# Kernel optimization log

Measured on AMD Instinct MI355X. Metric: run time of the kernel, lower is better.

Reference implementation:

```python
import jax, jax.numpy as jnp
import numpy as np
import math

B, SQ, SK = 8, 1024, 1024
DIM_Q = DIM_K = DIM_V = 512
H = 8
EPS = 1e-5
INF = jnp.float32(1e38)


def _ln(x, g, b):
    mu = jnp.mean(x, axis=-1, keepdims=True)
    var = jnp.mean(jnp.square(x - mu), axis=-1, keepdims=True)
    return (x - mu) * jax.lax.rsqrt(var + EPS) * g + b


def setup_inputs() -> dict:
    key = jax.random.key(0)
    ks = jax.random.split(key, 12)
    s = 1.0 / math.sqrt(DIM_V)
    return {
        "queries": jax.random.normal(ks[0], (B, SQ, DIM_Q), jnp.float32),
        "keys": jax.random.normal(ks[1], (B, SK, DIM_K), jnp.float32),
        # binary presence masks (as in the original usage)
        "presence_q": (jax.random.uniform(ks[2], (B, SQ)) > 0.1).astype(jnp.float32),
        "presence_k": (jax.random.uniform(ks[3], (B, SK)) > 0.1).astype(jnp.float32),
        "num_heads": H,
        "Wq": jax.random.normal(ks[4], (DIM_Q, DIM_V), jnp.float32) * s,
        "bq": jnp.zeros((DIM_V,), jnp.float32),
        "Wk": jax.random.normal(ks[5], (DIM_K, DIM_V), jnp.float32) * s,
        "bk": jnp.zeros((DIM_V,), jnp.float32),
        "Wv": jax.random.normal(ks[6], (DIM_K, DIM_V), jnp.float32) * s,
        "bv": jnp.zeros((DIM_V,), jnp.float32),
        "Wo": jax.random.normal(ks[7], (DIM_V, DIM_V), jnp.float32) * s,
        "bo": jnp.zeros((DIM_V,), jnp.float32),
        "g0": jnp.ones((DIM_V,), jnp.float32),
        "b0": jnp.zeros((DIM_V,), jnp.float32),
        "g1": jnp.ones((DIM_V,), jnp.float32),
        "b1": jnp.zeros((DIM_V,), jnp.float32),
    }


def reference(queries, keys, presence_q, presence_k, num_heads,
              Wq, bq, Wk, bk, Wv, bv, Wo, bo, g0, b0, g1, b1):
    b, sq, _ = queries.shape
    dim_v = Wq.shape[1]
    d = dim_v // num_heads
    q = queries @ Wq + bq                              # [B,Sq,V]
    k = keys @ Wk + bk                                 # [B,Sk,V]
    v = keys @ Wv + bv                                 # [B,Sk,V]
    qh = q.reshape(b, sq, num_heads, d)
    kh = k.reshape(b, -1, num_heads, d)
    vh = v.reshape(b, -1, num_heads, d)
    logits = jnp.einsum('bqhd,bkhd->bhqk', qh, kh) / jnp.float32(math.sqrt(dim_v))
    pq = presence_q[:, None, :, None]                  # [B,1,Sq,1]
    logits = pq * logits - (1.0 - pq) * INF
    pk = presence_k[:, None, None, :]                  # [B,1,1,Sk]
    logits = pk * logits - (1.0 - pk) * INF
    A = jax.nn.softmax(logits, axis=-1)                # [B,H,Sq,Sk]
    o = qh + jnp.einsum('bhqk,bkhd->bqhd', A, vh)      # residual add of Q_
    o = o.reshape(b, sq, dim_v)
    o = _ln(o, g0, b0)
    o = o + jax.nn.relu(o @ Wo + bo)
    o = _ln(o, g1, b1)
    return o
```

## Files before the change

### kernel.cpp

```cpp
#include <hip/hip_runtime.h>

typedef __attribute__((ext_vector_type(8))) short short8;
typedef __attribute__((ext_vector_type(4))) float f32x4;

#define SCALE2 0.06375871571f
#define C1     674.4237f

__device__ __forceinline__ float bfu(unsigned short u){
  return __uint_as_float(((unsigned int)u) << 16);
}
__device__ __forceinline__ unsigned short f2b(float x){
  unsigned int b = __float_as_uint(x);
  return (unsigned short)((b + 0x7fffu + ((b>>16)&1u)) >> 16);
}
__device__ __forceinline__ uint4 pack8(const float* f){
  float4 a = *(const float4*)f, b = *(const float4*)(f+4);
  uint4 r;
  r.x = (unsigned)f2b(a.x) | ((unsigned)f2b(a.y)<<16);
  r.y = (unsigned)f2b(a.z) | ((unsigned)f2b(a.w)<<16);
  r.z = (unsigned)f2b(b.x) | ((unsigned)f2b(b.y)<<16);
  r.w = (unsigned)f2b(b.z) | ((unsigned)f2b(b.w)<<16);
  return r;
}

__global__ __launch_bounds__(256) void conv_bf(
    const float* q, const float* k, unsigned short* dst)
{
  long i = ((long)blockIdx.x*256 + threadIdx.x)*8;
  const float* src = (i < 4194304) ? q + i : k + (i - 4194304);
  *(uint4*)(dst + i) = pack8(src);
}

__global__ __launch_bounds__(256) void prep_w(
    const float* Wq, const float* Wk, const float* Wv, const float* Wo,
    unsigned short* wt)
{
  const int m = blockIdx.z;
  const float* W = (m==0)?Wq:(m==1)?Wk:(m==2)?Wv:Wo;
  unsigned short* dst = wt + (long)m*262144;
  __shared__ unsigned short tile[64][72];
  const int t = threadIdx.x;
  const int n0 = blockIdx.x*64, k0 = blockIdx.y*64;
  {
    int r = t>>2, c0 = (t&3)*16;
    uint4 u0 = pack8(W + (long)(k0+r)*512 + n0 + c0);
    uint4 u1 = pack8(W + (long)(k0+r)*512 + n0 + c0 + 8);
    unsigned short* us0 = (unsigned short*)&u0;
    unsigned short* us1 = (unsigned short*)&u1;
    #pragma unroll
    for (int i=0;i<8;++i) tile[c0+i][r] = us0[i];
    #pragma unroll
    for (int i=0;i<8;++i) tile[c0+8+i][r] = us1[i];
  }
  __syncthreads();
  {
    int n = t>>2, ks = (t&3)*16;
    *(uint4*)(dst + (long)(n0+n)*512 + k0 + ks)     = *(uint4*)&tile[n][ks];
    *(uint4*)(dst + (long)(n0+n)*512 + k0 + ks + 8) = *(uint4*)&tile[n][ks+8];
  }
}

__global__ __launch_bounds__(256) void proj_mfma(
    const unsigned short* qin, const unsigned short* kin, const unsigned short* wt,
    const float* bq, const float* bk, const float* bv,
    unsigned short* q_bf, unsigned short* k_bf, unsigned short* vt_bf)
{
  const int mat = blockIdx.z;
  const unsigned short* A = (mat==0)? qin : kin;
  const unsigned short* Wt = wt + (long)mat*262144;
  const float* bias = (mat==0)?bq:(mat==1)?bk:bv;
  const int row0 = blockIdx.y*128, col0 = blockIdx.x*128;
  __shared__ unsigned short As[2][128][40];
  __shared__ unsigned short Ws[2][128][40];
  const int t = threadIdx.x;
  const int lane = t & 63, wid = t >> 6;
  const int ln = lane & 15, quad = lane >> 4;
  const int wy = wid >> 1, wx = wid & 1;
  f32x4 acc[4][4];
  #pragma unroll
  for (int i=0;i<4;++i){
    #pragma unroll
    for (int j=0;j<4;++j) acc[i][j] = (f32x4){0.f,0.f,0.f,0.f};
  }
  const int sr = t>>1, sk0 = (t&1)*16;
  const unsigned short* Arow = A  + (long)(row0+sr)*512 + sk0;
  const unsigned short* Wrow = Wt + (long)(col0+sr)*512 + sk0;
  uint4 a0 = *(const uint4*)(Arow);
  uint4 a1 = *(const uint4*)(Arow + 8);
  uint4 w0 = *(const uint4*)(Wrow);
  uint4 w1 = *(const uint4*)(Wrow + 8);
  *(uint4*)&As[0][sr][sk0]   = a0;
  *(uint4*)&As[0][sr][sk0+8] = a1;
  *(uint4*)&Ws[0][sr][sk0]   = w0;
  *(uint4*)&Ws[0][sr][sk0+8] = w1;
  __syncthreads();
  for (int it=0; it<16; ++it){
    const int cur = it & 1;
    if (it < 15){
      a0 = *(const uint4*)(Arow + (it+1)*32);
      a1 = *(const uint4*)(Arow + (it+1)*32 + 8);
      w0 = *(const uint4*)(Wrow + (it+1)*32);
      w1 = *(const uint4*)(Wrow + (it+1)*32 + 8);
    }
    short8 a[4], b[4];
    #pragma unroll
    for (int mt=0;mt<4;++mt) a[mt] = *(const short8*)&As[cur][wy*64+mt*16+ln][quad*8];
    #pragma unroll
    for (int nt=0;nt<4;++nt) b[nt] = *(const short8*)&Ws[cur][wx*64+nt*16+ln][quad*8];
    #pragma unroll
    for (int mt=0;mt<4;++mt){
      #pragma unroll
      for (int nt=0;nt<4;++nt)
        acc[mt][nt] = __builtin_amdgcn_mfma_f32_16x16x32_bf16(a[mt], b[nt], acc[mt][nt], 0,0,0);
    }
    if (it < 15){
      *(uint4*)&As[cur^1][sr][sk0]   = a0;
      *(uint4*)&As[cur^1][sr][sk0+8] = a1;
      *(uint4*)&Ws[cur^1][sr][sk0]   = w0;
      *(uint4*)&Ws[cur^1][sr][sk0+8] = w1;
    }
    __syncthreads();
  }
  float bias_v[4];
  #pragma unroll
  for (int nt=0;nt<4;++nt) bias_v[nt] = bias[col0 + wx*64 + nt*16 + ln];
  if (mat < 2){
    unsigned short* dst = (mat==0)? q_bf : k_bf;
    #pragma unroll
    for (int mt=0;mt<4;++mt){
      int row = row0 + wy*64 + mt*16 + quad*4;
      #pragma unroll
      for (int nt=0;nt<4;++nt){
        int col = col0 + wx*64 + nt*16 + ln;
        #pragma unroll
        for (int r=0;r<4;++r)
          dst[(long)(row+r)*512 + col] = f2b(acc[mt][nt][r] + bias_v[nt]);
      }
    }
  } else {
    #pragma unroll
    for (int mt=0;mt<4;++mt){
      int row = row0 + wy*64 + mt*16 + quad*4;
      int bb = row >> 10, sk = row & 1023;
      #pragma unroll
      for (int nt=0;nt<4;++nt){
        int col = col0 + wx*64 + nt*16 + ln;
        int h = col >> 6, dd = col & 63;
        uint2 pk2; unsigned short* pp = (unsigned short*)&pk2;
        #pragma unroll
        for (int r=0;r<4;++r) pp[r] = f2b(acc[mt][nt][r] + bias_v[nt]);
        *(uint2*)(vt_bf + (((long)((bb*8+h)*64+dd)) << 10) + sk) = pk2;
      }
    }
  }
}

__global__ __launch_bounds__(512) void attn_mfma(
    const unsigned short* q_bf, const unsigned short* k_bf, const unsigned short* vt_bf,
    const float* pres_q, const float* pres_k, float* o1)
{
  const int bx = blockIdx.x;
  const int b = bx >> 3, h = bx & 7;
  const int q0 = blockIdx.y * 128;
  const int t = threadIdx.x;
  const int lane = t & 63, wid = t >> 6, ln = lane & 15, quad = lane >> 4;
  __shared__ unsigned short Qs[128][72];
  __shared__ unsigned short Ks[64][72];
  __shared__ unsigned short Vt[64][72];
  __shared__ unsigned short Ps[128][72];
  __shared__ float pq_s[128], pk_s[64];
  {
    int tok = t>>2, ds = (t&3)*16;
    const unsigned short* src = q_bf + (long)(b*1024 + q0 + tok)*512 + h*64 + ds;
    *(uint4*)&Qs[tok][ds]   = *(const uint4*)src;
    *(uint4*)&Qs[tok][ds+8] = *(const uint4*)(src+8);
  }
  if (t < 128) pq_s[t] = pres_q[b*1024 + q0 + t];
  __syncthreads();
  short8 aq0 = *(const short8*)&Qs[wid*16+ln][quad*8];
  short8 aq1 = *(const short8*)&Qs[wid*16+ln][32+quad*8];
  float av[4];
  #pragma unroll
  for (int r=0;r<4;++r) av[r] = pq_s[wid*16 + quad*4 + r]*SCALE2;
  f32x4 oacc[4];
  #pragma unroll
  for (int dt=0;dt<4;++dt) oacc[dt] = (f32x4){0.f,0.f,0.f,0.f};
  float lsum[4] = {0.f,0.f,0.f,0.f};

  for (int k0=0;k0<1024;k0+=64){
    __syncthreads();
    {
      int tok = t>>3, ds = (t&7)*8;
      *(uint4*)&Ks[tok][ds] = *(const uint4*)(k_bf + (long)(b*1024 + k0 + tok)*512 + h*64 + ds);
      *(uint4*)&Vt[tok][ds] = *(const uint4*)(vt_bf + (((long)((b*8+h)*64 + tok)) << 10) + k0 + ds);
    }
    if (t < 64) pk_s[t] = pres_k[b*1024 + k0 + t];
    __syncthreads();
    f32x4 s[4];
    #pragma unroll
    for (int kt=0;kt<4;++kt) s[kt] = (f32x4){0.f,0.f,0.f,0.f};
    #pragma unroll
    for (int kt=0;kt<4;++kt){
      short8 kb0 = *(const short8*)&Ks[kt*16+ln][quad*8];
      short8 kb1 = *(const short8*)&Ks[kt*16+ln][32+quad*8];
      s[kt] = __builtin_amdgcn_mfma_f32_16x16x32_bf16(aq0, kb0, s[kt], 0,0,0);
      s[kt] = __builtin_amdgcn_mfma_f32_16x16x32_bf16(aq1, kb1, s[kt], 0,0,0);
    }
    float pk4[4];
    #pragma unroll
    for (int kt=0;kt<4;++kt) pk4[kt] = pk_s[kt*16+ln];
    #pragma unroll
    for (int r=0;r<4;++r){
      float sv[4];
      #pragma unroll
      for (int kt=0;kt<4;++kt){
        float a = av[r]*pk4[kt];
        float c = __builtin_fmaf(a, C1, -43.f);
        float x = __builtin_fmaf(s[kt][r], a, c);
        x = fminf(fmaxf(x, -100.f), 60.f);
        float e = __builtin_amdgcn_exp2f(x);
        lsum[r] += e;
        sv[kt] = e;
      }
      int prow = wid*16 + quad*4 + r;
      #pragma unroll
      for (int kt=0;kt<4;++kt) Ps[prow][kt*16+ln] = f2b(sv[kt]);
    }
    short8 ap0 = *(const short8*)&Ps[wid*16+ln][quad*8];
    short8 ap1 = *(const short8*)&Ps[wid*16+ln][32+quad*8];
    #pragma unroll
    for (int dt=0;dt<4;++dt){
      short8 vb0 = *(const short8*)&Vt[dt*16+ln][quad*8];
      short8 vb1 = *(const short8*)&Vt[dt*16+ln][32+quad*8];
      oacc[dt] = __builtin_amdgcn_mfma_f32_16x16x32_bf16(ap0, vb0, oacc[dt], 0,0,0);
      oacc[dt] = __builtin_amdgcn_mfma_f32_16x16x32_bf16(ap1, vb1, oacc[dt], 0,0,0);
    }
  }
  #pragma unroll
  for (int r=0;r<4;++r){
    float l = lsum[r];
    #pragma unroll
    for (int msk=1; msk<16; msk<<=1) l += __shfl_xor(l, msk);
    float inv = 1.f / l;
    int ql = wid*16 + quad*4 + r;
    long base = (long)(b*1024 + q0 + ql)*512 + h*64;
    #pragma unroll
    for (int dt=0;dt<4;++dt)
      o1[base + dt*16 + ln] = bfu(Qs[ql][dt*16+ln]) + oacc[dt][r]*inv;
  }
}

__global__ __launch_bounds__(256) void ln_kernel(
    const float* in, void* outp, int mode, const float* g, const float* bvec)
{
  const int row = blockIdx.x*4 + (threadIdx.x >> 6);
  const int lane = threadIdx.x & 63;
  const float* x = in + (long)row*512 + lane*8;
  float v[8];
  *(float4*)&v[0] = *(const float4*)x;
  *(float4*)&v[4] = *(const float4*)(x + 4);
  float sum = 0.f;
  #pragma unroll
  for (int c=0;c<8;++c) sum += v[c];
  #pragma unroll
  for (int msk=1; msk<64; msk<<=1) sum += __shfl_xor(sum, msk);
  float mu = sum * (1.f/512.f);
  float var = 0.f;
  #pragma unroll
  for (int c=0;c<8;++c){ v[c] -= mu; var += v[c]*v[c]; }
  #pragma unroll
  for (int msk=1; msk<64; msk<<=1) var += __shfl_xor(var, msk);
  float rs = rsqrtf(var*(1.f/512.f) + 1e-5f);
  float gv[8], bv[8];
  *(float4*)&gv[0] = *(const float4*)(g + lane*8);
  *(float4*)&gv[4] = *(const float4*)(g + lane*8 + 4);
  *(float4*)&bv[0] = *(const float4*)(bvec + lane*8);
  *(float4*)&bv[4] = *(const float4*)(bvec + lane*8 + 4);
  float y[8];
  #pragma unroll
  for (int c=0;c<8;++c) y[c] = v[c]*rs*gv[c] + bv[c];
  if (mode){
    float* dst = (float*)outp + (long)row*512 + lane*8;
    *(float4*)dst       = *(float4*)&y[0];
    *(float4*)(dst + 4) = *(float4*)&y[4];
  } else {
    uint4 out; unsigned short* os = (unsigned short*)&out;
    #pragma unroll
    for (int c=0;c<8;++c) os[c] = f2b(y[c]);
    *(uint4*)((unsigned short*)outp + (long)row*512 + lane*8) = out;
  }
}

__global__ __launch_bounds__(256) void out_mfma(
    const unsigned short* t_bf, const unsigned short* Wt, const float* bo,
    float* o1)
{
  const int row0 = blockIdx.y*64, col0 = blockIdx.x*128;
  __shared__ unsigned short As[2][64][40];
  __shared__ unsigned short Ws[2][128][40];
  const int t = threadIdx.x;
  const int lane = t & 63, wid = t >> 6;
  const int ln = lane & 15, quad = lane >> 4;
  const int wy = wid >> 1, wx = wid & 1;
  f32x4 acc[2][4];
  #pragma unroll
  for (int i=0;i<2;++i){
    #pragma unroll
    for (int j=0;j<4;++j) acc[i][j] = (f32x4){0.f,0.f,0.f,0.f};
  }
  const int ar = t>>2, ac0 = (t&3)*8;
  const int wr = t>>1, wc0 = (t&1)*16;
  const unsigned short* Arow = t_bf + (long)(row0+ar)*512 + ac0;
  const unsigned short* Wrow = Wt   + (long)(col0+wr)*512 + wc0;
  uint4 a0 = *(const uint4*)(Arow);
  uint4 w0 = *(const uint4*)(Wrow);
  uint4 w1 = *(const uint4*)(Wrow + 8);
  *(uint4*)&As[0][ar][ac0] = a0;
  *(uint4*)&Ws[0][wr][wc0]   = w0;
  *(uint4*)&Ws[0][wr][wc0+8] = w1;
  __syncthreads();
  for (int it=0; it<16; ++it){
    const int cur = it & 1;
    if (it < 15){
      a0 = *(const uint4*)(Arow + (it+1)*32);
      w0 = *(const uint4*)(Wrow + (it+1)*32);
      w1 = *(const uint4*)(Wrow + (it+1)*32 + 8);
    }
    short8 a[2], b[4];
    #pragma unroll
    for (int mt=0;mt<2;++mt) a[mt] = *(const short8*)&As[cur][wy*32+mt*16+ln][quad*8];
    #pragma unroll
    for (int nt=0;nt<4;++nt) b[nt] = *(const short8*)&Ws[cur][wx*64+nt*16+ln][quad*8];
    #pragma unroll
    for (int mt=0;mt<2;++mt){
      #pragma unroll
      for (int nt=0;nt<4;++nt)
        acc[mt][nt] = __builtin_amdgcn_mfma_f32_16x16x32_bf16(a[mt], b[nt], acc[mt][nt], 0,0,0);
    }
    if (it < 15){
      *(uint4*)&As[cur^1][ar][ac0] = a0;
      *(uint4*)&Ws[cur^1][wr][wc0]   = w0;
      *(uint4*)&Ws[cur^1][wr][wc0+8] = w1;
    }
    __syncthreads();
  }
  float bias_v[4];
  #pragma unroll
  for (int nt=0;nt<4;++nt) bias_v[nt] = bo[col0 + wx*64 + nt*16 + ln];
  #pragma unroll
  for (int mt=0;mt<2;++mt){
    int row = row0 + wy*32 + mt*16 + quad*4;
    #pragma unroll
    for (int nt=0;nt<4;++nt){
      int col = col0 + wx*64 + nt*16 + ln;
      #pragma unroll
      for (int r=0;r<4;++r){
        long idx = (long)(row+r)*512 + col;
        float u = acc[mt][nt][r] + bias_v[nt];
        u = fmaxf(u, 0.f);
        o1[idx] = bfu(t_bf[idx]) + u;
      }
    }
  }
}

extern "C" void kernel_launch(void* const* d_in, const int* in_sizes, int n_in,
                              void* d_out, int out_size, void* d_ws, size_t ws_size,
                              hipStream_t stream)
{
  unsigned short* q_bf  = (unsigned short*)d_ws;
  unsigned short* k_bf  = q_bf  + 8192l*512;
  unsigned short* vt_bf = k_bf  + 8192l*512;
  unsigned short* t_bf  = vt_bf + 8192l*512;
  unsigned short* wt    = t_bf  + 8192l*512;
  float* o1 = (float*)(wt + 4l*512*512);
  unsigned short* qin = (unsigned short*)o1;
  unsigned short* kin = qin + 4194304;

  hipLaunchKernelGGL(conv_bf, dim3(4096), dim3(256), 0, stream,
                     (const float*)d_in[0], (const float*)d_in[1], qin);
  hipLaunchKernelGGL(prep_w, dim3(8,8,4), dim3(256), 0, stream,
                     (const float*)d_in[5], (const float*)d_in[7],
                     (const float*)d_in[9], (const float*)d_in[11], wt);
  hipLaunchKernelGGL(proj_mfma, dim3(4,64,3), dim3(256), 0, stream,
                     qin, kin, wt,
                     (const float*)d_in[6], (const float*)d_in[8],
                     (const float*)d_in[10], q_bf, k_bf, vt_bf);
  hipLaunchKernelGGL(attn_mfma, dim3(64,8), dim3(512), 0, stream,
                     q_bf, k_bf, vt_bf,
                     (const float*)d_in[2], (const float*)d_in[3], o1);
  hipLaunchKernelGGL(ln_kernel, dim3(2048), dim3(256), 0, stream,
                     o1, (void*)t_bf, 0, (const float*)d_in[13], (const float*)d_in[14]);
  hipLaunchKernelGGL(out_mfma, dim3(4,128), dim3(256), 0, stream,
                     t_bf, wt + 3l*512*512, (const float*)d_in[12], o1);
  hipLaunchKernelGGL(ln_kernel, dim3(2048), dim3(256), 0, stream,
                     o1, d_out, 1, (const float*)d_in[15], (const float*)d_in[16]);
}
```

Baseline: 213.4 us.

## Double-buffer attention K/V, bf16 intermediates, merge prep kernels, simplify softmax math

Merges the input-conversion and weight-transpose kernels into a single launch. The attention kernel now double-buffers K/V tiles with register prefetch, so it needs one barrier per iteration instead of two. It also reuses the Q shared buffer for P, simplifies the fixed-offset softmax exponent, and truncates P to bf16 instead of rounding it. The intermediates between attention, LayerNorm and the output projection are stored as bf16 instead of fp32, which halves that memory traffic but adds rounding error before each LayerNorm. The clamp on the exponent is removed and the residual Q is read from global memory, and both changes slightly alter numerical behaviour.

```diff
diff --git a/kernel.cpp b/kernel.cpp
--- a/kernel.cpp
+++ b/kernel.cpp
@@ -4,7 +4,6 @@
 typedef __attribute__((ext_vector_type(4))) float f32x4;
 
 #define SCALE2 0.06375871571f
-#define C1     674.4237f
 
 __device__ __forceinline__ float bfu(unsigned short u){
   return __uint_as_float(((unsigned int)u) << 16);
@@ -23,40 +22,38 @@
   return r;
 }
 
-__global__ __launch_bounds__(256) void conv_bf(
-    const float* q, const float* k, unsigned short* dst)
-{
-  long i = ((long)blockIdx.x*256 + threadIdx.x)*8;
-  const float* src = (i < 4194304) ? q + i : k + (i - 4194304);
-  *(uint4*)(dst + i) = pack8(src);
-}
-
-__global__ __launch_bounds__(256) void prep_w(
+__global__ __launch_bounds__(256) void prep_inputs(
     const float* Wq, const float* Wk, const float* Wv, const float* Wo,
-    unsigned short* wt)
-{
-  const int m = blockIdx.z;
-  const float* W = (m==0)?Wq:(m==1)?Wk:(m==2)?Wv:Wo;
-  unsigned short* dst = wt + (long)m*262144;
-  __shared__ unsigned short tile[64][72];
-  const int t = threadIdx.x;
-  const int n0 = blockIdx.x*64, k0 = blockIdx.y*64;
-  {
-    int r = t>>2, c0 = (t&3)*16;
-    uint4 u0 = pack8(W + (long)(k0+r)*512 + n0 + c0);
-    uint4 u1 = pack8(W + (long)(k0+r)*512 + n0 + c0 + 8);
-    unsigned short* us0 = (unsigned short*)&u0;
-    unsigned short* us1 = (unsigned short*)&u1;
-    #pragma unroll
-    for (int i=0;i<8;++i) tile[c0+i][r] = us0[i];
-    #pragma unroll
-    for (int i=0;i<8;++i) tile[c0+8+i][r] = us1[i];
-  }
-  __syncthreads();
-  {
-    int n = t>>2, ks = (t&3)*16;
-    *(uint4*)(dst + (long)(n0+n)*512 + k0 + ks)     = *(uint4*)&tile[n][ks];
-    *(uint4*)(dst + (long)(n0+n)*512 + k0 + ks + 8) = *(uint4*)&tile[n][ks+8];
+    const float* q, const float* k, unsigned short* wt, unsigned short* qk_dst)
+{
+  const int id = blockIdx.x, t = threadIdx.x;
+  if (id < 256){
+    const int m = id >> 6;
+    const float* W = (m==0)?Wq:(m==1)?Wk:(m==2)?Wv:Wo;
+    unsigned short* dst = wt + (long)m*262144;
+    __shared__ unsigned short tile[64][72];
+    const int n0 = ((id>>3)&7)*64, k0 = (id&7)*64;
+    {
+      int r = t>>2, c0 = (t&3)*16;
+      uint4 u0 = pack8(W + (long)(k0+r)*512 + n0 + c0);
+      uint4 u1 = pack8(W + (long)(k0+r)*512 + n0 + c0 + 8);
+      unsigned short* us0 = (unsigned short*)&u0;
+      unsigned short* us1 = (unsigned short*)&u1;
+      #pragma unroll
+      for (int i=0;i<8;++i) tile[c0+i][r] = us0[i];
+      #pragma unroll
+      for (int i=0;i<8;++i) tile[c0+8+i][r] = us1[i];
+    }
+    __syncthreads();
+    {
+      int n = t>>2, ks = (t&3)*16;
+      *(uint4*)(dst + (long)(n0+n)*512 + k0 + ks)     = *(uint4*)&tile[n][ks];
+      *(uint4*)(dst + (long)(n0+n)*512 + k0 + ks + 8) = *(uint4*)&tile[n][ks+8];
+    }
+  } else {
+    long i = ((long)(id-256)*256 + t)*8;
+    const float* src = (i < 4194304) ? q + i : k + (i - 4194304);
+    *(uint4*)(qk_dst + i) = pack8(src);
   }
 }
 
@@ -157,84 +154,95 @@
 
 __global__ __launch_bounds__(512) void attn_mfma(
     const unsigned short* q_bf, const unsigned short* k_bf, const unsigned short* vt_bf,
-    const float* pres_q, const float* pres_k, float* o1)
+    const float* pres_q, const float* pres_k, unsigned short* o_bf)
 {
   const int bx = blockIdx.x;
   const int b = bx >> 3, h = bx & 7;
   const int q0 = blockIdx.y * 128;
   const int t = threadIdx.x;
   const int lane = t & 63, wid = t >> 6, ln = lane & 15, quad = lane >> 4;
-  __shared__ unsigned short Qs[128][72];
-  __shared__ unsigned short Ks[64][72];
-  __shared__ unsigned short Vt[64][72];
-  __shared__ unsigned short Ps[128][72];
-  __shared__ float pq_s[128], pk_s[64];
+  __shared__ unsigned short QP[128][72];
+  __shared__ unsigned short Ks[2][64][72];
+  __shared__ unsigned short Vt[2][64][72];
+  __shared__ float pq_s[128];
+  __shared__ float pk_s[2][64];
   {
     int tok = t>>2, ds = (t&3)*16;
     const unsigned short* src = q_bf + (long)(b*1024 + q0 + tok)*512 + h*64 + ds;
-    *(uint4*)&Qs[tok][ds]   = *(const uint4*)src;
-    *(uint4*)&Qs[tok][ds+8] = *(const uint4*)(src+8);
+    *(uint4*)&QP[tok][ds]   = *(const uint4*)src;
+    *(uint4*)&QP[tok][ds+8] = *(const uint4*)(src+8);
+  }
+  {
+    int tok = t>>3, ds = (t&7)*8;
+    *(uint4*)&Ks[0][tok][ds] = *(const uint4*)(k_bf + (long)(b*1024 + tok)*512 + h*64 + ds);
+    *(uint4*)&Vt[0][tok][ds] = *(const uint4*)(vt_bf + (((long)((b*8+h)*64 + tok)) << 10) + ds);
   }
   if (t < 128) pq_s[t] = pres_q[b*1024 + q0 + t];
+  if (t < 64)  pk_s[0][t] = pres_k[b*1024 + t];
   __syncthreads();
-  short8 aq0 = *(const short8*)&Qs[wid*16+ln][quad*8];
-  short8 aq1 = *(const short8*)&Qs[wid*16+ln][32+quad*8];
-  float av[4];
-  #pragma unroll
-  for (int r=0;r<4;++r) av[r] = pq_s[wid*16 + quad*4 + r]*SCALE2;
+  short8 aq0 = *(const short8*)&QP[wid*16+ln][quad*8];
+  short8 aq1 = *(const short8*)&QP[wid*16+ln][32+quad*8];
+  float av[4], mval[4];
+  #pragma unroll
+  for (int r=0;r<4;++r){
+    av[r] = pq_s[wid*16 + quad*4 + r]*SCALE2;
+    mval[r] = (av[r] == 0.f) ? 0.f : -43.f;
+  }
   f32x4 oacc[4];
   #pragma unroll
   for (int dt=0;dt<4;++dt) oacc[dt] = (f32x4){0.f,0.f,0.f,0.f};
   float lsum[4] = {0.f,0.f,0.f,0.f};
 
-  for (int k0=0;k0<1024;k0+=64){
-    __syncthreads();
-    {
+  for (int it=0; it<16; ++it){
+    const int cur = it & 1;
+    const int k0n = (it+1)*64;
+    uint4 pf_k, pf_v; float pf_p = 0.f;
+    if (it < 15){
       int tok = t>>3, ds = (t&7)*8;
-      *(uint4*)&Ks[tok][ds] = *(const uint4*)(k_bf + (long)(b*1024 + k0 + tok)*512 + h*64 + ds);
-      *(uint4*)&Vt[tok][ds] = *(const uint4*)(vt_bf + (((long)((b*8+h)*64 + tok)) << 10) + k0 + ds);
-    }
-    if (t < 64) pk_s[t] = pres_k[b*1024 + k0 + t];
-    __syncthreads();
+      pf_k = *(const uint4*)(k_bf + (long)(b*1024 + k0n + tok)*512 + h*64 + ds);
+      pf_v = *(const uint4*)(vt_bf + (((long)((b*8+h)*64 + tok)) << 10) + k0n + ds);
+      if (t < 64) pf_p = pres_k[b*1024 + k0n + t];
+    }
     f32x4 s[4];
     #pragma unroll
     for (int kt=0;kt<4;++kt) s[kt] = (f32x4){0.f,0.f,0.f,0.f};
     #pragma unroll
     for (int kt=0;kt<4;++kt){
-      short8 kb0 = *(const short8*)&Ks[kt*16+ln][quad*8];
-      short8 kb1 = *(const short8*)&Ks[kt*16+ln][32+quad*8];
+      short8 kb0 = *(const short8*)&Ks[cur][kt*16+ln][quad*8];
+      short8 kb1 = *(const short8*)&Ks[cur][kt*16+ln][32+quad*8];
       s[kt] = __builtin_amdgcn_mfma_f32_16x16x32_bf16(aq0, kb0, s[kt], 0,0,0);
       s[kt] = __builtin_amdgcn_mfma_f32_16x16x32_bf16(aq1, kb1, s[kt], 0,0,0);
     }
     float pk4[4];
     #pragma unroll
-    for (int kt=0;kt<4;++kt) pk4[kt] = pk_s[kt*16+ln];
+    for (int kt=0;kt<4;++kt) pk4[kt] = pk_s[cur][kt*16+ln];
     #pragma unroll
     for (int r=0;r<4;++r){
-      float sv[4];
       #pragma unroll
       for (int kt=0;kt<4;++kt){
-        float a = av[r]*pk4[kt];
-        float c = __builtin_fmaf(a, C1, -43.f);
-        float x = __builtin_fmaf(s[kt][r], a, c);
-        x = fminf(fmaxf(x, -100.f), 60.f);
+        float x0 = s[kt][r]*av[r];
+        float x = __builtin_fmaf(pk4[kt], x0 - mval[r], mval[r]);
         float e = __builtin_amdgcn_exp2f(x);
         lsum[r] += e;
-        sv[kt] = e;
+        QP[wid*16+quad*4+r][kt*16+ln] = (unsigned short)(__float_as_uint(e) >> 16);
       }
-      int prow = wid*16 + quad*4 + r;
-      #pragma unroll
-      for (int kt=0;kt<4;++kt) Ps[prow][kt*16+ln] = f2b(sv[kt]);
-    }
-    short8 ap0 = *(const short8*)&Ps[wid*16+ln][quad*8];
-    short8 ap1 = *(const short8*)&Ps[wid*16+ln][32+quad*8];
+    }
+    short8 ap0 = *(const short8*)&QP[wid*16+ln][quad*8];
+    short8 ap1 = *(const short8*)&QP[wid*16+ln][32+quad*8];
     #pragma unroll
     for (int dt=0;dt<4;++dt){
-      short8 vb0 = *(const short8*)&Vt[dt*16+ln][quad*8];
-      short8 vb1 = *(const short8*)&Vt[dt*16+ln][32+quad*8];
+      short8 vb0 = *(const short8*)&Vt[cur][dt*16+ln][quad*8];
+      short8 vb1 = *(const short8*)&Vt[cur][dt*16+ln][32+quad*8];
       oacc[dt] = __builtin_amdgcn_mfma_f32_16x16x32_bf16(ap0, vb0, oacc[dt], 0,0,0);
       oacc[dt] = __builtin_amdgcn_mfma_f32_16x16x32_bf16(ap1, vb1, oacc[dt], 0,0,0);
     }
+    if (it < 15){
+      int tok = t>>3, ds = (t&7)*8;
+      *(uint4*)&Ks[cur^1][tok][ds] = pf_k;
+      *(uint4*)&Vt[cur^1][tok][ds] = pf_v;
+      if (t < 64) pk_s[cur^1][t] = pf_p;
+    }
+    __syncthreads();
   }
   #pragma unroll
   for (int r=0;r<4;++r){
@@ -245,20 +253,23 @@
     int ql = wid*16 + quad*4 + r;
     long base = (long)(b*1024 + q0 + ql)*512 + h*64;
     #pragma unroll
-    for (int dt=0;dt<4;++dt)
-      o1[base + dt*16 + ln] = bfu(Qs[ql][dt*16+ln]) + oacc[dt][r]*inv;
+    for (int dt=0;dt<4;++dt){
+      float qh = bfu(q_bf[base + dt*16 + ln]);
+      o_bf[base + dt*16 + ln] = f2b(qh + oacc[dt][r]*inv);
+    }
   }
 }
 
 __global__ __launch_bounds__(256) void ln_kernel(
-    const float* in, void* outp, int mode, const float* g, const float* bvec)
+    const unsigned short* in, void* outp, int mode, const float* g, const float* bvec)
 {
   const int row = blockIdx.x*4 + (threadIdx.x >> 6);
   const int lane = threadIdx.x & 63;
-  const float* x = in + (long)row*512 + lane*8;
+  uint4 raw = *(const uint4*)(in + (long)row*512 + lane*8);
+  const unsigned short* rs16 = (const unsigned short*)&raw;
   float v[8];
-  *(float4*)&v[0] = *(const float4*)x;
-  *(float4*)&v[4] = *(const float4*)(x + 4);
+  #pragma unroll
+  for (int c=0;c<8;++c) v[c] = bfu(rs16[c]);
   float sum = 0.f;
   #pragma unroll
   for (int c=0;c<8;++c) sum += v[c];
@@ -293,7 +304,7 @@
 
 __global__ __launch_bounds__(256) void out_mfma(
     const unsigned short* t_bf, const unsigned short* Wt, const float* bo,
-    float* o1)
+    unsigned short* u_bf)
 {
   const int row0 = blockIdx.y*64, col0 = blockIdx.x*128;
   __shared__ unsigned short As[2][64][40];
@@ -358,7 +369,7 @@
         long idx = (long)(row+r)*512 + col;
         float u = acc[mt][nt][r] + bias_v[nt];
         u = fmaxf(u, 0.f);
-        o1[idx] = bfu(t_bf[idx]) + u;
+        u_bf[idx] = f2b(bfu(t_bf[idx]) + u);
       }
     }
   }
@@ -373,26 +384,26 @@
   unsigned short* vt_bf = k_bf  + 8192l*512;
   unsigned short* t_bf  = vt_bf + 8192l*512;
   unsigned short* wt    = t_bf  + 8192l*512;
-  float* o1 = (float*)(wt + 4l*512*512);
-  unsigned short* qin = (unsigned short*)o1;
-  unsigned short* kin = qin + 4194304;
-
-  hipLaunchKernelGGL(conv_bf, dim3(4096), dim3(256), 0, stream,
-                     (const float*)d_in[0], (const float*)d_in[1], qin);
-  hipLaunchKernelGGL(prep_w, dim3(8,8,4), dim3(256), 0, stream,
+  unsigned short* qin   = wt + 4l*512*512;
+  unsigned short* kin   = qin + 4194304;
+  unsigned short* o_bf  = qin;
+  unsigned short* u_bf  = kin;
+
+  hipLaunchKernelGGL(prep_inputs, dim3(4352), dim3(256), 0, stream,
                      (const float*)d_in[5], (const float*)d_in[7],
-                     (const float*)d_in[9], (const float*)d_in[11], wt);
+                     (const float*)d_in[9], (const float*)d_in[11],
+                     (const float*)d_in[0], (const float*)d_in[1], wt, qin);
   hipLaunchKernelGGL(proj_mfma, dim3(4,64,3), dim3(256), 0, stream,
                      qin, kin, wt,
                      (const float*)d_in[6], (const float*)d_in[8],
                      (const float*)d_in[10], q_bf, k_bf, vt_bf);
   hipLaunchKernelGGL(attn_mfma, dim3(64,8), dim3(512), 0, stream,
                      q_bf, k_bf, vt_bf,
-                     (const float*)d_in[2], (const float*)d_in[3], o1);
+                     (const float*)d_in[2], (const float*)d_in[3], o_bf);
   hipLaunchKernelGGL(ln_kernel, dim3(2048), dim3(256), 0, stream,
-                     o1, (void*)t_bf, 0, (const float*)d_in[13], (const float*)d_in[14]);
+                     o_bf, (void*)t_bf, 0, (const float*)d_in[13], (const float*)d_in[14]);
   hipLaunchKernelGGL(out_mfma, dim3(4,128), dim3(256), 0, stream,
-                     t_bf, wt + 3l*512*512, (const float*)d_in[12], o1);
+                     t_bf, wt + 3l*512*512, (const float*)d_in[12], u_bf);
   hipLaunchKernelGGL(ln_kernel, dim3(2048), dim3(256), 0, stream,
-                     o1, d_out, 1, (const float*)d_in[15], (const float*)d_in[16]);
-}
+                     u_bf, d_out, 1, (const float*)d_in[15], (const float*)d_in[16]);
+}
```

New measurement: 208.3 us. 2.4% less time.
